# Optimization experiments

Measured on AMD Instinct MI355X. Metric: run time of the kernel, lower is better.

The kernel has to match this reference:

```python
import jax, jax.numpy as jnp
import numpy as np

B, INDIM, ENC, BOT, DEC = 2048, 20000, 512, 128, 512
EPS = 1e-5


def _bn(x, g, b):
    # BatchNorm1d in training mode: biased batch stats
    m = jnp.mean(x, axis=0)
    v = jnp.mean(jnp.square(x - m), axis=0)
    return (x - m) * jax.lax.rsqrt(v + EPS) * g + b


def setup_inputs() -> dict:
    key = jax.random.key(0)
    ks = jax.random.split(key, 8)
    s = 0.02  # small init scale keeps exp() outputs finite
    return {
        "x": jax.random.uniform(ks[0], (B, INDIM), dtype=jnp.float32),
        "bn0_g": jnp.ones((INDIM,), jnp.float32),
        "bn0_b": jnp.zeros((INDIM,), jnp.float32),
        "enc_W": jax.random.normal(ks[1], (ENC, INDIM), jnp.float32) * s,
        "enc_b": jnp.zeros((ENC,), jnp.float32),
        "bn1_g": jnp.ones((ENC,), jnp.float32),
        "bn1_b": jnp.zeros((ENC,), jnp.float32),
        "bot_W": jax.random.normal(ks[2], (BOT, ENC), jnp.float32) * s,
        "bot_b": jnp.zeros((BOT,), jnp.float32),
        "bn2_g": jnp.ones((BOT,), jnp.float32),
        "bn2_b": jnp.zeros((BOT,), jnp.float32),
        "dec_W": jax.random.normal(ks[3], (DEC, BOT), jnp.float32) * s,
        "dec_b": jnp.zeros((DEC,), jnp.float32),
        "o1_W": jax.random.normal(ks[4], (INDIM, DEC), jnp.float32) * s,
        "o1_b": jnp.zeros((INDIM,), jnp.float32),
        "o2_W": jax.random.normal(ks[5], (INDIM, DEC), jnp.float32) * s,
        "o2_b": jnp.zeros((INDIM,), jnp.float32),
        "o3_W": jax.random.normal(ks[6], (INDIM, DEC), jnp.float32) * s,
        "o3_b": jnp.zeros((INDIM,), jnp.float32),
    }


def reference(x, bn0_g, bn0_b, enc_W, enc_b, bn1_g, bn1_b, bot_W, bot_b,
              bn2_g, bn2_b, dec_W, dec_b, o1_W, o1_b, o2_W, o2_b, o3_W, o3_b):
    # row-sum / median normalization; diag-inverse @ x == x / s[:, None]
    row_sum = jnp.sum(x, axis=1)                     # [B]
    s = row_sum / jnp.median(row_sum)                # [B]
    h = jnp.log1p(x / s[:, None])                    # log(inv(diag(s)) @ x + 1)
    h = _bn(h, bn0_g, bn0_b)
    h = jax.nn.relu(h @ enc_W.T + enc_b)
    h = _bn(h, bn1_g, bn1_b)
    h = jax.nn.relu(h @ bot_W.T + bot_b)
    h = _bn(h, bn2_g, bn2_b)
    h = jax.nn.relu(h @ dec_W.T + dec_b)
    M = jnp.exp(h @ o1_W.T + o1_b)
    M_loss = s[:, None] * M                          # diag(s) @ M
    pai = jax.nn.sigmoid(h @ o2_W.T + o2_b)
    theta = jnp.exp(h @ o3_W.T + o3_b)
    return pai, M, theta, M_loss
```

## Files before the change

### kernel.cpp

```cpp
#include <hip/hip_runtime.h>
#include <hip/hip_bf16.h>
#include <math.h>

#define B_    2048
#define IND   20000
#define ENCN  512
#define BOTN  128
#define DECN  512
#define KP1   20480
#define NP    20224
#define SPLITK 16
#define KSTEP1 20
#define BNEPS 1e-5f

typedef __hip_bfloat16 bf16;
typedef __bf16 bf16x8 __attribute__((ext_vector_type(8)));
typedef float f32x4 __attribute__((ext_vector_type(4)));
typedef unsigned short u16;

__device__ __forceinline__ u16 f2bfu(float f) {
  __hip_bfloat16 h = __float2bfloat16(f);
  return *reinterpret_cast<u16*>(&h);
}

__device__ __forceinline__ void gload_lds16(const bf16* g, bf16* l) {
  __builtin_amdgcn_global_load_lds(
      (const __attribute__((address_space(1))) void*)g,
      (__attribute__((address_space(3))) void*)l, 16, 0, 0);
}

__global__ void rowsum_k(const float* __restrict__ x, float* __restrict__ row_sum) {
  const int row = blockIdx.x;
  const f32x4* xr = (const f32x4*)(x + (size_t)row * IND);
  float s = 0.f;
  for (int i = threadIdx.x; i < IND / 4; i += 256) {
    f32x4 v = xr[i];
    s += (v[0] + v[1]) + (v[2] + v[3]);
  }
#pragma unroll
  for (int o = 32; o > 0; o >>= 1) s += __shfl_down(s, o, 64);
  __shared__ float ws4[4];
  if ((threadIdx.x & 63) == 0) ws4[threadIdx.x >> 6] = s;
  __syncthreads();
  if (threadIdx.x == 0) row_sum[row] = (ws4[0] + ws4[1]) + (ws4[2] + ws4[3]);
}

__global__ void median_scale_k(const float* __restrict__ row_sum,
                               float* __restrict__ sArr, float* __restrict__ invs) {
  __shared__ float v[B_];
  const int tid = threadIdx.x;
  v[tid] = row_sum[tid];
  v[tid + 1024] = row_sum[tid + 1024];
  __syncthreads();
  for (int k = 2; k <= B_; k <<= 1) {
    for (int j = k >> 1; j > 0; j >>= 1) {
      for (int i = tid; i < B_; i += 1024) {
        int ixj = i ^ j;
        if (ixj > i) {
          bool up = ((i & k) == 0);
          float a = v[i], b = v[ixj];
          if ((a > b) == up) { v[i] = b; v[ixj] = a; }
        }
      }
      __syncthreads();
    }
  }
  float med = 0.5f * (v[B_ / 2 - 1] + v[B_ / 2]);
  for (int i = tid; i < B_; i += 1024) {
    float rs = row_sum[i];
    sArr[i] = rs / med;
    invs[i] = med / rs;
  }
}

__global__ void pass2_k(const float* __restrict__ x, const float* __restrict__ invs,
                        bf16* __restrict__ L, float* __restrict__ part_s,
                        float* __restrict__ part_q) {
  const int c0 = (blockIdx.x * 256 + threadIdx.x) * 4;
  const int rblk = blockIdx.y;
  const int r0 = rblk * 32;
  const bool valid = (c0 < IND);
  f32x4 sum = {0.f, 0.f, 0.f, 0.f}, sq = {0.f, 0.f, 0.f, 0.f};
  for (int r = r0; r < r0 + 32; ++r) {
    f32x4 lv = {0.f, 0.f, 0.f, 0.f};
    if (valid) {
      f32x4 v = *(const f32x4*)(x + (size_t)r * IND + c0);
      float iv = invs[r];
      lv[0] = log1pf(v[0] * iv); lv[1] = log1pf(v[1] * iv);
      lv[2] = log1pf(v[2] * iv); lv[3] = log1pf(v[3] * iv);
      sum += lv; sq += lv * lv;
    }
    ushort4 o;
    o.x = f2bfu(lv[0]); o.y = f2bfu(lv[1]); o.z = f2bfu(lv[2]); o.w = f2bfu(lv[3]);
    *(ushort4*)((u16*)L + (size_t)r * KP1 + c0) = o;
  }
  if (valid) {
    *(f32x4*)(part_s + (size_t)rblk * KP1 + c0) = sum;
    *(f32x4*)(part_q + (size_t)rblk * KP1 + c0) = sq;
  }
}

__global__ void finalize_bn_k(const float* __restrict__ part_s, const float* __restrict__ part_q,
                              const float* __restrict__ g, const float* __restrict__ b,
                              float* __restrict__ scale, float* __restrict__ shift) {
  int c = blockIdx.x * 256 + threadIdx.x;
  if (c >= IND) return;
  float s = 0.f, q = 0.f;
  for (int z = 0; z < 64; ++z) {
    s += part_s[(size_t)z * KP1 + c];
    q += part_q[(size_t)z * KP1 + c];
  }
  const float invN = 1.f / (float)B_;
  float mean = s * invN;
  float var = q * invN - mean * mean;
  float sc = g[c] * rsqrtf(var + BNEPS);
  scale[c] = sc;
  shift[c] = b[c] - mean * sc;
}

__global__ void prepw_k(const float* __restrict__ encW, const float* __restrict__ enc_b,
                        const float* __restrict__ scale0, const float* __restrict__ shift0,
                        bf16* __restrict__ Wp, float* __restrict__ bias1) {
  const int e = blockIdx.x;
  float local = 0.f;
  for (int j0 = threadIdx.x * 4; j0 < KP1; j0 += 1024) {
    ushort4 o;
    if (j0 < IND) {
      f32x4 w = *(const f32x4*)(encW + (size_t)e * IND + j0);
      f32x4 sc = *(const f32x4*)(scale0 + j0);
      f32x4 sh = *(const f32x4*)(shift0 + j0);
      local += sh[0] * w[0] + sh[1] * w[1] + sh[2] * w[2] + sh[3] * w[3];
      o.x = f2bfu(w[0] * sc[0]); o.y = f2bfu(w[1] * sc[1]);
      o.z = f2bfu(w[2] * sc[2]); o.w = f2bfu(w[3] * sc[3]);
    } else {
      o.x = 0; o.y = 0; o.z = 0; o.w = 0;
    }
    *(ushort4*)((u16*)Wp + (size_t)e * KP1 + j0) = o;
  }
#pragma unroll
  for (int o = 32; o > 0; o >>= 1) local += __shfl_down(local, o, 64);
  __shared__ float red[4];
  if ((threadIdx.x & 63) == 0) red[threadIdx.x >> 6] = local;
  __syncthreads();
  if (threadIdx.x == 0) bias1[e] = enc_b[e] + ((red[0] + red[1]) + (red[2] + red[3]));
}

template <int MODE>
__global__ __launch_bounds__(512, 2)
void gemm256(const bf16* __restrict__ A, const bf16* __restrict__ Bm,
             int Kpad, int ksteps,
             float* __restrict__ out0, float* __restrict__ out1,
             const float* __restrict__ bias, const float* __restrict__ sArr,
             int ldo, int Nlimit) {
  extern __shared__ __align__(16) bf16 smem[];
  bf16* Asm = smem;
  bf16* Bsm = smem + 32768;
  const int tid = threadIdx.x;
  const int lane = tid & 63;
  const int wave = tid >> 6;
  const int wr = wave >> 2;
  const int wc = wave & 3;

  const int nwg = gridDim.x;
  const int q8 = nwg >> 3;
  const int bid = blockIdx.x;
  const int swz = (bid & 7) * q8 + (bid >> 3);
  const int xm = swz & 7;
  const int rest = swz >> 3;
  int yn, z;
  if (MODE == 0) { yn = rest & 1; z = rest >> 1; } else { yn = rest; z = 0; }
  const int m0 = xm * 256;
  const int n0 = yn * 256;
  const int kbeg = z * ksteps * 64;

  const int srow = tid >> 3;
  const int schunk = (tid & 7) ^ (srow & 7);
  const bf16* gA = A + (size_t)(m0 + srow) * Kpad + kbeg + schunk * 8;
  const bf16* gB = Bm + (size_t)(n0 + srow) * Kpad + kbeg + schunk * 8;
  const int dst1 = tid * 8;

  const int lrow = lane & 15;
  const int kq = lane >> 4;
  const int rsw = lrow & 7;

  f32x4 acc[8][4] = {};
  bf16x8 bfv[4][2];

  auto SA = [&](int kt, int half) {
    const bf16* g = gA + (size_t)(half * 128) * Kpad + (size_t)kt * 64;
    bf16* l = Asm + (((kt & 1) * 2 + half) << 13) + dst1;
    gload_lds16(g, l);
    gload_lds16(g + (size_t)64 * Kpad, l + 4096);
  };
  auto SB = [&](int kt, int half) {
    const bf16* g = gB + (size_t)(half * 128) * Kpad + (size_t)kt * 64;
    bf16* l = Bsm + (((kt & 1) * 2 + half) << 13) + dst1;
    gload_lds16(g, l);
    gload_lds16(g + (size_t)64 * Kpad, l + 4096);
  };
  auto DSA = [&](int slot, int p, bf16x8 af[2][2]) {
#pragma unroll
    for (int i = 0; i < 2; ++i) {
      const int m = 2 * p + i;
      const int base = ((slot * 2 + (m >> 2)) * 128 + (m & 3) * 32 + wr * 16 + lrow) * 64;
#pragma unroll
      for (int kk = 0; kk < 2; ++kk)
        af[i][kk] = *(const bf16x8*)(&Asm[base + (((kk * 4 + kq) ^ rsw) << 3)]);
    }
  };
  auto DSB = [&](int slot) {
#pragma unroll
    for (int n = 0; n < 4; ++n) {
      const int base = ((slot * 2 + (wc >> 1)) * 128 + (wc & 1) * 64 + n * 16 + lrow) * 64;
#pragma unroll
      for (int kk = 0; kk < 2; ++kk)
        bfv[n][kk] = *(const bf16x8*)(&Bsm[base + (((kk * 4 + kq) ^ rsw) << 3)]);
    }
  };
  auto MF = [&](int p, bf16x8 af[2][2]) {
    __builtin_amdgcn_s_setprio(1);
#pragma unroll
    for (int i = 0; i < 2; ++i)
#pragma unroll
      for (int n = 0; n < 4; ++n)
#pragma unroll
        for (int kk = 0; kk < 2; ++kk)
          acc[2 * p + i][n] = __builtin_amdgcn_mfma_f32_16x16x32_bf16(
              bfv[n][kk], af[i][kk], acc[2 * p + i][n], 0, 0, 0);
    __builtin_amdgcn_s_setprio(0);
  };

  SA(0, 0); SA(0, 1); SB(0, 0); SB(0, 1);
  SB(1, 0); SB(1, 1); SA(1, 0);
  asm volatile("s_waitcnt vmcnt(6)" ::: "memory");
  __builtin_amdgcn_s_barrier();

  const int iters = ksteps >> 1;
  for (int t = 0; t < iters; ++t) {
    const int e = 2 * t;
    const bool last = (t == iters - 1);
    bf16x8 af[2][2];
    DSB(0); DSA(0, 0, af);
    SA(e + 1, 1);
    __builtin_amdgcn_s_barrier();
    MF(0, af);
    __builtin_amdgcn_s_barrier();
    DSA(0, 1, af);
    if (!last) SB(e + 2, 0);
    __builtin_amdgcn_s_barrier();
    MF(1, af);
    __builtin_amdgcn_s_barrier();
    DSA(0, 2, af);
    if (!last) SB(e + 2, 1);
    __builtin_amdgcn_s_barrier();
    MF(2, af);
    __builtin_amdgcn_s_barrier();
    DSA(0, 3, af);
    if (!last) SA(e + 2, 0);
    if (last) { asm volatile("s_waitcnt vmcnt(0)" ::: "memory"); }
    else      { asm volatile("s_waitcnt vmcnt(6)" ::: "memory"); }
    __builtin_amdgcn_s_barrier();
    MF(3, af);
    __builtin_amdgcn_s_barrier();
    DSB(1); DSA(1, 0, af);
    if (!last) SA(e + 2, 1);
    __builtin_amdgcn_s_barrier();
    MF(0, af);
    __builtin_amdgcn_s_barrier();
    DSA(1, 1, af);
    if (!last) SB(e + 3, 0);
    __builtin_amdgcn_s_barrier();
    MF(1, af);
    __builtin_amdgcn_s_barrier();
    DSA(1, 2, af);
    if (!last) SB(e + 3, 1);
    __builtin_amdgcn_s_barrier();
    MF(2, af);
    __builtin_amdgcn_s_barrier();
    DSA(1, 3, af);
    if (!last) SA(e + 3, 0);
    if (last) { asm volatile("s_waitcnt vmcnt(0)" ::: "memory"); }
    else      { asm volatile("s_waitcnt vmcnt(6)" ::: "memory"); }
    __builtin_amdgcn_s_barrier();
    MF(3, af);
    __builtin_amdgcn_s_barrier();
  }

  float* o0 = out0;
  if (MODE == 0) o0 += (size_t)z * ((size_t)B_ * ldo);
  const int gcolb = n0 + wc * 64 + kq * 4;
#pragma unroll
  for (int m = 0; m < 8; ++m) {
    const int grow = m0 + m * 32 + wr * 16 + lrow;
    float srow_s = 0.f;
    if (MODE == 2) srow_s = sArr[grow];
#pragma unroll
    for (int n = 0; n < 4; ++n) {
      const int gcol = gcolb + n * 16;
      f32x4 v = acc[m][n];
      if (MODE == 0) {
        *(f32x4*)(&o0[(size_t)grow * ldo + gcol]) = v;
      } else if (gcol < Nlimit) {
        f32x4 bb = *(const f32x4*)(&bias[gcol]);
        f32x4 t = v + bb;
        f32x4 r;
        if (MODE == 1) {
#pragma unroll
          for (int j = 0; j < 4; ++j) r[j] = 1.f / (1.f + __expf(-t[j]));
          *(f32x4*)(&o0[(size_t)grow * ldo + gcol]) = r;
        } else if (MODE == 2) {
#pragma unroll
          for (int j = 0; j < 4; ++j) r[j] = __expf(t[j]);
          *(f32x4*)(&o0[(size_t)grow * ldo + gcol]) = r;
          f32x4 rl;
#pragma unroll
          for (int j = 0; j < 4; ++j) rl[j] = srow_s * r[j];
          *(f32x4*)(&out1[(size_t)grow * ldo + gcol]) = rl;
        } else {
#pragma unroll
          for (int j = 0; j < 4; ++j) r[j] = __expf(t[j]);
          *(f32x4*)(&o0[(size_t)grow * ldo + gcol]) = r;
        }
      }
    }
  }
}

template <int MODE>
__global__ __launch_bounds__(256, 2)
void gemm128(const bf16* __restrict__ A, const bf16* __restrict__ Bm,
             int Kpad, int ksteps,
             float* __restrict__ outF, bf16* __restrict__ outB,
             const float* __restrict__ bias, int ldo) {
  __shared__ __align__(16) bf16 As[2][128 * 64];
  __shared__ __align__(16) bf16 Bs[2][128 * 64];
  const int tid = threadIdx.x;
  const int wave = tid >> 6;
  const int lane = tid & 63;
  const int wr = wave >> 1, wc = wave & 1;
  const int m0 = blockIdx.x * 128;
  const int n0 = blockIdx.y * 128;

  const int srow = wave * 32 + (lane >> 3);
  const int scol = ((lane & 7) ^ (lane >> 3)) * 8;
  const bf16* gA = A + (size_t)(m0 + srow) * Kpad + scol;
  const bf16* gB = Bm + (size_t)(n0 + srow) * Kpad + scol;
  const int lbase = wave * 2048;

  f32x4 acc[4][4] = {};
  const int lrow = lane & 15;
  const int swz = lrow & 7;
  const int kq = lane >> 4;

  auto STAGE = [&](int ks, int buf) {
    const bf16* ga = gA + (size_t)ks * 64;
    const bf16* gb = gB + (size_t)ks * 64;
#pragma unroll
    for (int i = 0; i < 4; ++i) {
      gload_lds16(ga + (size_t)(i * 8) * Kpad, &As[buf][lbase + i * 512]);
      gload_lds16(gb + (size_t)(i * 8) * Kpad, &Bs[buf][lbase + i * 512]);
    }
  };

  STAGE(0, 0);
  asm volatile("s_waitcnt vmcnt(0)" ::: "memory");
  __builtin_amdgcn_s_barrier();

  int cur = 0;
  for (int ks = 0; ks < ksteps; ++ks) {
    if (ks + 1 < ksteps) STAGE(ks + 1, cur ^ 1);
#pragma unroll
    for (int kk = 0; kk < 2; ++kk) {
      const int kc = kk * 4 + kq;
      bf16x8 af[4], bfv[4];
#pragma unroll
      for (int m = 0; m < 4; ++m) {
        const int row = wr * 64 + m * 16 + lrow;
        af[m] = *(const bf16x8*)(&As[cur][row * 64 + (((kc ^ swz) & 7) << 3)]);
      }
#pragma unroll
      for (int n = 0; n < 4; ++n) {
        const int row = wc * 64 + n * 16 + lrow;
        bfv[n] = *(const bf16x8*)(&Bs[cur][row * 64 + (((kc ^ swz) & 7) << 3)]);
      }
#pragma unroll
      for (int m = 0; m < 4; ++m)
#pragma unroll
        for (int n = 0; n < 4; ++n)
          acc[m][n] = __builtin_amdgcn_mfma_f32_16x16x32_bf16(bfv[n], af[m], acc[m][n], 0, 0, 0);
    }
    if (ks + 1 < ksteps) {
      asm volatile("s_waitcnt vmcnt(0)" ::: "memory");
      __builtin_amdgcn_s_barrier();
      cur ^= 1;
    }
  }

  const int growb = m0 + wr * 64 + lrow;
  const int gcolb = n0 + wc * 64 + kq * 4;
#pragma unroll
  for (int m = 0; m < 4; ++m) {
    const int grow = growb + m * 16;
#pragma unroll
    for (int n = 0; n < 4; ++n) {
      const int gcol = gcolb + n * 16;
      f32x4 bb = *(const f32x4*)(&bias[gcol]);
      f32x4 t = acc[m][n] + bb;
      if (MODE == 4) {
        f32x4 r;
#pragma unroll
        for (int j = 0; j < 4; ++j) r[j] = fmaxf(t[j], 0.f);
        *(f32x4*)(&outF[(size_t)grow * ldo + gcol]) = r;
      } else {
        ushort4 o;
        o.x = f2bfu(fmaxf(t[0], 0.f)); o.y = f2bfu(fmaxf(t[1], 0.f));
        o.z = f2bfu(fmaxf(t[2], 0.f)); o.w = f2bfu(fmaxf(t[3], 0.f));
        *(ushort4*)((u16*)outB + (size_t)grow * ldo + gcol) = o;
      }
    }
  }
}

__global__ void reduce1_k(const float* __restrict__ Cp, const float* __restrict__ bias1,
                          float* __restrict__ C1) {
  const size_t i4 = ((size_t)blockIdx.x * 256 + threadIdx.x) * 4;
  f32x4 t = {0.f, 0.f, 0.f, 0.f};
#pragma unroll
  for (int z = 0; z < SPLITK; ++z) t += *(const f32x4*)(Cp + (size_t)z * (B_ * ENCN) + i4);
  f32x4 bb = *(const f32x4*)(bias1 + (i4 & (ENCN - 1)));
  t += bb;
  f32x4 r;
#pragma unroll
  for (int j = 0; j < 4; ++j) r[j] = fmaxf(t[j], 0.f);
  *(f32x4*)(C1 + i4) = r;
}

__global__ void colpart_k(const float* __restrict__ X, int C,
                          float* __restrict__ ps, float* __restrict__ pq) {
  const int cl = threadIdx.x & 63;
  const int rg = threadIdx.x >> 6;
  const int c = blockIdx.x * 64 + cl;
  const int r0 = blockIdx.y * 64 + rg * 16;
  float sum = 0.f, sq = 0.f;
  for (int rr = 0; rr < 16; ++rr) {
    float v = X[(size_t)(r0 + rr) * C + c];
    sum += v; sq += v * v;
  }
  __shared__ float ls[4][64], lq[4][64];
  ls[rg][cl] = sum; lq[rg][cl] = sq;
  __syncthreads();
  if (rg == 0) {
    sum = (ls[0][cl] + ls[1][cl]) + (ls[2][cl] + ls[3][cl]);
    sq = (lq[0][cl] + lq[1][cl]) + (lq[2][cl] + lq[3][cl]);
    ps[(size_t)blockIdx.y * C + c] = sum;
    pq[(size_t)blockIdx.y * C + c] = sq;
  }
}

__global__ void colfin_k(const float* __restrict__ ps, const float* __restrict__ pq,
                         const float* __restrict__ g, const float* __restrict__ b,
                         float* __restrict__ scale, float* __restrict__ shift, int C) {
  int c = blockIdx.x * 256 + threadIdx.x;
  if (c >= C) return;
  float sum = 0.f, sq = 0.f;
  for (int z = 0; z < 32; ++z) {
    sum += ps[(size_t)z * C + c];
    sq += pq[(size_t)z * C + c];
  }
  const float invN = 1.f / (float)B_;
  float mean = sum * invN;
  float var = sq * invN - mean * mean;
  float sc = g[c] * rsqrtf(var + BNEPS);
  scale[c] = sc;
  shift[c] = b[c] - mean * sc;
}

__global__ void affine_k(const float* __restrict__ X, const float* __restrict__ sc,
                         const float* __restrict__ sh, bf16* __restrict__ out, int Cm1) {
  const size_t i4 = ((size_t)blockIdx.x * 256 + threadIdx.x) * 4;
  const int c0 = (int)(i4 & (size_t)Cm1);
  f32x4 v = *(const f32x4*)(X + i4);
  f32x4 s = *(const f32x4*)(sc + c0);
  f32x4 h = *(const f32x4*)(sh + c0);
  f32x4 t = v * s + h;
  ushort4 o;
  o.x = f2bfu(t[0]); o.y = f2bfu(t[1]); o.z = f2bfu(t[2]); o.w = f2bfu(t[3]);
  *(ushort4*)((u16*)out + i4) = o;
}

__global__ void cvtw_k(const float* __restrict__ src, bf16* __restrict__ dst) {
  const size_t i4 = ((size_t)blockIdx.x * 256 + threadIdx.x) * 4;
  f32x4 v = *(const f32x4*)(src + i4);
  ushort4 o;
  o.x = f2bfu(v[0]); o.y = f2bfu(v[1]); o.z = f2bfu(v[2]); o.w = f2bfu(v[3]);
  *(ushort4*)((u16*)dst + i4) = o;
}

__global__ void cvt_o_k(const float* __restrict__ Wsrc, bf16* __restrict__ Wb) {
  const size_t idx = ((size_t)blockIdx.x * 256 + threadIdx.x) * 4;
  const int e = (int)(idx >> 9);
  ushort4 o;
  if (e < IND) {
    f32x4 v = *(const f32x4*)(Wsrc + idx);
    o.x = f2bfu(v[0]); o.y = f2bfu(v[1]); o.z = f2bfu(v[2]); o.w = f2bfu(v[3]);
  } else {
    o.x = 0; o.y = 0; o.z = 0; o.w = 0;
  }
  *(ushort4*)((u16*)Wb + idx) = o;
}

extern "C" void kernel_launch(void* const* d_in, const int* in_sizes, int n_in,
                              void* d_out, int out_size, void* d_ws, size_t ws_size,
                              hipStream_t stream) {
  const float* x     = (const float*)d_in[0];
  const float* bn0_g = (const float*)d_in[1];
  const float* bn0_b = (const float*)d_in[2];
  const float* enc_W = (const float*)d_in[3];
  const float* enc_b = (const float*)d_in[4];
  const float* bn1_g = (const float*)d_in[5];
  const float* bn1_b = (const float*)d_in[6];
  const float* bot_W = (const float*)d_in[7];
  const float* bot_b = (const float*)d_in[8];
  const float* bn2_g = (const float*)d_in[9];
  const float* bn2_b = (const float*)d_in[10];
  const float* dec_W = (const float*)d_in[11];
  const float* dec_b = (const float*)d_in[12];
  const float* o1_W  = (const float*)d_in[13];
  const float* o1_b  = (const float*)d_in[14];
  const float* o2_W  = (const float*)d_in[15];
  const float* o2_b  = (const float*)d_in[16];
  const float* o3_W  = (const float*)d_in[17];
  const float* o3_b  = (const float*)d_in[18];

  char* wsb = (char*)d_ws;
  size_t off = 0;
  auto alloc = [&](size_t bytes) -> void* {
    void* p = wsb + off;
    off = (off + bytes + 255) & ~(size_t)255;
    return p;
  };
  float* row_sum = (float*)alloc(B_ * 4);
  float* sArr    = (float*)alloc(B_ * 4);
  float* invs    = (float*)alloc(B_ * 4);
  float* scale0  = (float*)alloc(IND * 4);
  float* shift0  = (float*)alloc(IND * 4);
  float* bias1   = (float*)alloc(ENCN * 4);
  float* scale1  = (float*)alloc(ENCN * 4);
  float* shift1  = (float*)alloc(ENCN * 4);
  float* scale2  = (float*)alloc(BOTN * 4);
  float* shift2  = (float*)alloc(BOTN * 4);
  float* ps1     = (float*)alloc(32 * ENCN * 4);
  float* pq1     = (float*)alloc(32 * ENCN * 4);
  float* ps2     = (float*)alloc(32 * BOTN * 4);
  float* pq2     = (float*)alloc(32 * BOTN * 4);
  float* C1      = (float*)alloc((size_t)B_ * ENCN * 4);
  float* C2f     = (float*)alloc((size_t)B_ * BOTN * 4);
  float* Cp      = (float*)alloc((size_t)SPLITK * B_ * ENCN * 4);
  bf16*  L       = (bf16*)alloc((size_t)B_ * KP1 * 2);
  bf16*  Wp      = (bf16*)alloc((size_t)ENCN * KP1 * 2);
  bf16*  A1b     = (bf16*)alloc((size_t)B_ * ENCN * 2);
  bf16*  A2b     = (bf16*)alloc((size_t)B_ * BOTN * 2);
  bf16*  botWb   = (bf16*)alloc((size_t)BOTN * ENCN * 2);
  bf16*  decWb   = (bf16*)alloc((size_t)DECN * BOTN * 2);
  bf16*  h3      = (bf16*)alloc((size_t)B_ * DECN * 2);
  bf16*  wbf0    = (bf16*)alloc((size_t)NP * 512 * 2);
  bf16*  wbf1    = (bf16*)alloc((size_t)NP * 512 * 2);
  bf16*  wbf2    = (bf16*)alloc((size_t)NP * 512 * 2);
  float* part_s  = Cp;
  float* part_q  = Cp + (size_t)64 * KP1;

  hipFuncSetAttribute(reinterpret_cast<const void*>(gemm256<0>),
                      hipFuncAttributeMaxDynamicSharedMemorySize, 131072);
  hipFuncSetAttribute(reinterpret_cast<const void*>(gemm256<1>),
                      hipFuncAttributeMaxDynamicSharedMemorySize, 131072);
  hipFuncSetAttribute(reinterpret_cast<const void*>(gemm256<2>),
                      hipFuncAttributeMaxDynamicSharedMemorySize, 131072);
  hipFuncSetAttribute(reinterpret_cast<const void*>(gemm256<3>),
                      hipFuncAttributeMaxDynamicSharedMemorySize, 131072);

  rowsum_k<<<B_, 256, 0, stream>>>(x, row_sum);
  median_scale_k<<<1, 1024, 0, stream>>>(row_sum, sArr, invs);

  pass2_k<<<dim3(KP1 / 1024, 64), 256, 0, stream>>>(x, invs, L, part_s, part_q);
  finalize_bn_k<<<(IND + 255) / 256, 256, 0, stream>>>(part_s, part_q, bn0_g, bn0_b,
                                                       scale0, shift0);

  prepw_k<<<ENCN, 256, 0, stream>>>(enc_W, enc_b, scale0, shift0, Wp, bias1);

  gemm256<0><<<8 * 2 * SPLITK, 512, 131072, stream>>>(
      L, Wp, KP1, KSTEP1, Cp, nullptr, nullptr, nullptr, ENCN, ENCN);
  reduce1_k<<<(B_ * ENCN) / 1024, 256, 0, stream>>>(Cp, bias1, C1);

  colpart_k<<<dim3(ENCN / 64, 32), 256, 0, stream>>>(C1, ENCN, ps1, pq1);
  colfin_k<<<2, 256, 0, stream>>>(ps1, pq1, bn1_g, bn1_b, scale1, shift1, ENCN);
  affine_k<<<(B_ * ENCN) / 1024, 256, 0, stream>>>(C1, scale1, shift1, A1b, ENCN - 1);
  cvtw_k<<<(BOTN * ENCN) / 1024, 256, 0, stream>>>(bot_W, botWb);
  gemm128<4><<<dim3(16, 1), 256, 0, stream>>>(A1b, botWb, ENCN, ENCN / 64,
                                              C2f, nullptr, bot_b, BOTN);
  colpart_k<<<dim3(BOTN / 64, 32), 256, 0, stream>>>(C2f, BOTN, ps2, pq2);
  colfin_k<<<1, 256, 0, stream>>>(ps2, pq2, bn2_g, bn2_b, scale2, shift2, BOTN);
  affine_k<<<(B_ * BOTN) / 1024, 256, 0, stream>>>(C2f, scale2, shift2, A2b, BOTN - 1);
  cvtw_k<<<(DECN * BOTN) / 1024, 256, 0, stream>>>(dec_W, decWb);
  gemm128<5><<<dim3(16, 4), 256, 0, stream>>>(A2b, decWb, BOTN, BOTN / 64,
                                              nullptr, h3, dec_b, DECN);

  const int cvtg = (NP * 512) / 1024;
  cvt_o_k<<<cvtg, 256, 0, stream>>>(o1_W, wbf0);
  cvt_o_k<<<cvtg, 256, 0, stream>>>(o2_W, wbf1);
  cvt_o_k<<<cvtg, 256, 0, stream>>>(o3_W, wbf2);

  float* out = (float*)d_out;
  const size_t OFF = (size_t)B_ * IND;
  const int onwg = 8 * (NP / 256);
  gemm256<1><<<onwg, 512, 131072, stream>>>(
      h3, wbf1, 512, 8, out, nullptr, o2_b, nullptr, IND, IND);
  gemm256<2><<<onwg, 512, 131072, stream>>>(
      h3, wbf0, 512, 8, out + OFF, out + 3 * OFF, o1_b, sArr, IND, IND);
  gemm256<3><<<onwg, 512, 131072, stream>>>(
      h3, wbf2, 512, 8, out + 2 * OFF, nullptr, o3_b, nullptr, IND, IND);
}
```

Baseline: 670.8 us.

## Fuse three output GEMMs into one persistent kernel with cross-tile prefetch

Result: slower. 710.0 us (+5.8%).

```diff
diff --git a/kernel.cpp b/kernel.cpp
--- a/kernel.cpp
+++ b/kernel.cpp
@@ -145,13 +145,9 @@
   if (threadIdx.x == 0) bias1[e] = enc_b[e] + ((red[0] + red[1]) + (red[2] + red[3]));
 }
 
-template <int MODE>
 __global__ __launch_bounds__(512, 2)
-void gemm256(const bf16* __restrict__ A, const bf16* __restrict__ Bm,
-             int Kpad, int ksteps,
-             float* __restrict__ out0, float* __restrict__ out1,
-             const float* __restrict__ bias, const float* __restrict__ sArr,
-             int ldo, int Nlimit) {
+void gemm1_k(const bf16* __restrict__ A, const bf16* __restrict__ Bm,
+             float* __restrict__ Cp) {
   extern __shared__ __align__(16) bf16 smem[];
   bf16* Asm = smem;
   bf16* Bsm = smem + 32768;
@@ -161,22 +157,20 @@
   const int wr = wave >> 2;
   const int wc = wave & 3;
 
-  const int nwg = gridDim.x;
-  const int q8 = nwg >> 3;
   const int bid = blockIdx.x;
-  const int swz = (bid & 7) * q8 + (bid >> 3);
+  const int swz = (bid & 7) * 32 + (bid >> 3);
   const int xm = swz & 7;
   const int rest = swz >> 3;
-  int yn, z;
-  if (MODE == 0) { yn = rest & 1; z = rest >> 1; } else { yn = rest; z = 0; }
+  const int yn = rest & 1;
+  const int z = rest >> 1;
   const int m0 = xm * 256;
   const int n0 = yn * 256;
-  const int kbeg = z * ksteps * 64;
+  const int kbeg = z * KSTEP1 * 64;
 
   const int srow = tid >> 3;
   const int schunk = (tid & 7) ^ (srow & 7);
-  const bf16* gA = A + (size_t)(m0 + srow) * Kpad + kbeg + schunk * 8;
-  const bf16* gB = Bm + (size_t)(n0 + srow) * Kpad + kbeg + schunk * 8;
+  const bf16* gA = A + (size_t)(m0 + srow) * KP1 + kbeg + schunk * 8;
+  const bf16* gB = Bm + (size_t)(n0 + srow) * KP1 + kbeg + schunk * 8;
   const int dst1 = tid * 8;
 
   const int lrow = lane & 15;
@@ -187,16 +181,16 @@
   bf16x8 bfv[4][2];
 
   auto SA = [&](int kt, int half) {
-    const bf16* g = gA + (size_t)(half * 128) * Kpad + (size_t)kt * 64;
+    const bf16* g = gA + (size_t)(half * 128) * KP1 + (size_t)kt * 64;
     bf16* l = Asm + (((kt & 1) * 2 + half) << 13) + dst1;
     gload_lds16(g, l);
-    gload_lds16(g + (size_t)64 * Kpad, l + 4096);
+    gload_lds16(g + (size_t)64 * KP1, l + 4096);
   };
   auto SB = [&](int kt, int half) {
-    const bf16* g = gB + (size_t)(half * 128) * Kpad + (size_t)kt * 64;
+    const bf16* g = gB + (size_t)(half * 128) * KP1 + (size_t)kt * 64;
     bf16* l = Bsm + (((kt & 1) * 2 + half) << 13) + dst1;
     gload_lds16(g, l);
-    gload_lds16(g + (size_t)64 * Kpad, l + 4096);
+    gload_lds16(g + (size_t)64 * KP1, l + 4096);
   };
   auto DSA = [&](int slot, int p, bf16x8 af[2][2]) {
 #pragma unroll
@@ -235,7 +229,7 @@
   asm volatile("s_waitcnt vmcnt(6)" ::: "memory");
   __builtin_amdgcn_s_barrier();
 
-  const int iters = ksteps >> 1;
+  const int iters = KSTEP1 >> 1;
   for (int t = 0; t < iters; ++t) {
     const int e = 2 * t;
     const bool last = (t == iters - 1);
@@ -286,42 +280,220 @@
     __builtin_amdgcn_s_barrier();
   }
 
-  float* o0 = out0;
-  if (MODE == 0) o0 += (size_t)z * ((size_t)B_ * ldo);
+  float* o0 = Cp + (size_t)z * ((size_t)B_ * ENCN);
   const int gcolb = n0 + wc * 64 + kq * 4;
 #pragma unroll
   for (int m = 0; m < 8; ++m) {
     const int grow = m0 + m * 32 + wr * 16 + lrow;
-    float srow_s = 0.f;
-    if (MODE == 2) srow_s = sArr[grow];
 #pragma unroll
     for (int n = 0; n < 4; ++n) {
       const int gcol = gcolb + n * 16;
-      f32x4 v = acc[m][n];
-      if (MODE == 0) {
-        *(f32x4*)(&o0[(size_t)grow * ldo + gcol]) = v;
-      } else if (gcol < Nlimit) {
-        f32x4 bb = *(const f32x4*)(&bias[gcol]);
-        f32x4 t = v + bb;
-        f32x4 r;
-        if (MODE == 1) {
-#pragma unroll
-          for (int j = 0; j < 4; ++j) r[j] = 1.f / (1.f + __expf(-t[j]));
-          *(f32x4*)(&o0[(size_t)grow * ldo + gcol]) = r;
-        } else if (MODE == 2) {
-#pragma unroll
-          for (int j = 0; j < 4; ++j) r[j] = __expf(t[j]);
-          *(f32x4*)(&o0[(size_t)grow * ldo + gcol]) = r;
-          f32x4 rl;
-#pragma unroll
-          for (int j = 0; j < 4; ++j) rl[j] = srow_s * r[j];
-          *(f32x4*)(&out1[(size_t)grow * ldo + gcol]) = rl;
-        } else {
-#pragma unroll
-          for (int j = 0; j < 4; ++j) r[j] = __expf(t[j]);
-          *(f32x4*)(&o0[(size_t)grow * ldo + gcol]) = r;
+      *(f32x4*)(&o0[(size_t)grow * ENCN + gcol]) = acc[m][n];
+    }
+  }
+}
+
+__global__ __launch_bounds__(512, 2)
+void gemm_outp_k(const bf16* __restrict__ A,
+                 const bf16* __restrict__ W0, const bf16* __restrict__ W1,
+                 const bf16* __restrict__ W2,
+                 const float* __restrict__ b0, const float* __restrict__ b1,
+                 const float* __restrict__ b2,
+                 const float* __restrict__ sArr, float* __restrict__ out) {
+  extern __shared__ __align__(16) bf16 smem[];
+  bf16* Asm = smem;
+  bf16* Bsm = smem + 32768;
+  const int tid = threadIdx.x;
+  const int lane = tid & 63;
+  const int wave = tid >> 6;
+  const int wr = wave >> 2;
+  const int wc = wave & 3;
+
+  const int bid = blockIdx.x;
+  const int c = bid & 7;
+  const int j = bid >> 3;
+  const int nt = (j < 13) ? 8 : 7;
+
+  const int srow = tid >> 3;
+  const int schunk = (tid & 7) ^ (srow & 7);
+  const int dst1 = tid * 8;
+  const int lrow = lane & 15;
+  const int kq = lane >> 4;
+  const int rsw = lrow & 7;
+  const size_t OFF = (size_t)B_ * IND;
+
+  const int xm = (c * 237 + j) & 7;
+  const int m0 = xm * 256;
+  const bf16* gA = A + (size_t)(m0 + srow) * ENCN + schunk * 8;
+
+  auto tileParams = [&](int it, int& g, int& yn) {
+    const int tg = c * 237 + j + 32 * it;
+    g = tg / 632;
+    yn = (tg - g * 632) >> 3;
+  };
+  auto wsel = [&](int g) -> const bf16* { return (g == 0) ? W0 : (g == 1) ? W1 : W2; };
+
+  int g_cur, yn_cur;
+  tileParams(0, g_cur, yn_cur);
+  const bf16* gB_cur = wsel(g_cur) + (size_t)(yn_cur * 256 + srow) * ENCN + schunk * 8;
+  int g_nxt = 0, yn_nxt = 0;
+  const bf16* gB_nxt = gB_cur;
+  if (nt > 1) {
+    tileParams(1, g_nxt, yn_nxt);
+    gB_nxt = wsel(g_nxt) + (size_t)(yn_nxt * 256 + srow) * ENCN + schunk * 8;
+  }
+
+  f32x4 acc[8][4] = {};
+  bf16x8 bfv[4][2];
+
+  auto SA = [&](int kt, int half) {
+    const bf16* g = gA + (size_t)(half * 128) * ENCN + (size_t)(kt & 7) * 64;
+    bf16* l = Asm + (((kt & 1) * 2 + half) << 13) + dst1;
+    gload_lds16(g, l);
+    gload_lds16(g + (size_t)64 * ENCN, l + 4096);
+  };
+  auto SB = [&](int kt, int half) {
+    const bf16* base = (kt >= 8) ? gB_nxt : gB_cur;
+    const bf16* g = base + (size_t)(half * 128) * ENCN + (size_t)(kt & 7) * 64;
+    bf16* l = Bsm + (((kt & 1) * 2 + half) << 13) + dst1;
+    gload_lds16(g, l);
+    gload_lds16(g + (size_t)64 * ENCN, l + 4096);
+  };
+  auto DSA = [&](int slot, int p, bf16x8 af[2][2]) {
+#pragma unroll
+    for (int i = 0; i < 2; ++i) {
+      const int m = 2 * p + i;
+      const int base = ((slot * 2 + (m >> 2)) * 128 + (m & 3) * 32 + wr * 16 + lrow) * 64;
+#pragma unroll
+      for (int kk = 0; kk < 2; ++kk)
+        af[i][kk] = *(const bf16x8*)(&Asm[base + (((kk * 4 + kq) ^ rsw) << 3)]);
+    }
+  };
+  auto DSB = [&](int slot) {
+#pragma unroll
+    for (int n = 0; n < 4; ++n) {
+      const int base = ((slot * 2 + (wc >> 1)) * 128 + (wc & 1) * 64 + n * 16 + lrow) * 64;
+#pragma unroll
+      for (int kk = 0; kk < 2; ++kk)
+        bfv[n][kk] = *(const bf16x8*)(&Bsm[base + (((kk * 4 + kq) ^ rsw) << 3)]);
+    }
+  };
+  auto MF = [&](int p, bf16x8 af[2][2]) {
+    __builtin_amdgcn_s_setprio(1);
+#pragma unroll
+    for (int i = 0; i < 2; ++i)
+#pragma unroll
+      for (int n = 0; n < 4; ++n)
+#pragma unroll
+        for (int kk = 0; kk < 2; ++kk)
+          acc[2 * p + i][n] = __builtin_amdgcn_mfma_f32_16x16x32_bf16(
+              bfv[n][kk], af[i][kk], acc[2 * p + i][n], 0, 0, 0);
+    __builtin_amdgcn_s_setprio(0);
+  };
+
+  SA(0, 0); SA(0, 1); SB(0, 0); SB(0, 1);
+  SB(1, 0); SB(1, 1); SA(1, 0);
+  asm volatile("s_waitcnt vmcnt(6)" ::: "memory");
+  __builtin_amdgcn_s_barrier();
+
+  for (int it = 0; it < nt; ++it) {
+    const bool lastTile = (it == nt - 1);
+#pragma unroll 1
+    for (int t = 0; t < 4; ++t) {
+      const int e = 2 * t;
+      const bool last = lastTile && (t == 3);
+      bf16x8 af[2][2];
+      DSB(0); DSA(0, 0, af);
+      SA(e + 1, 1);
+      __builtin_amdgcn_s_barrier();
+      MF(0, af);
+      __builtin_amdgcn_s_barrier();
+      DSA(0, 1, af);
+      if (!last) SB(e + 2, 0);
+      __builtin_amdgcn_s_barrier();
+      MF(1, af);
+      __builtin_amdgcn_s_barrier();
+      DSA(0, 2, af);
+      if (!last) SB(e + 2, 1);
+      __builtin_amdgcn_s_barrier();
+      MF(2, af);
+      __builtin_amdgcn_s_barrier();
+      DSA(0, 3, af);
+      if (!last) SA(e + 2, 0);
+      if (last) { asm volatile("s_waitcnt vmcnt(0)" ::: "memory"); }
+      else      { asm volatile("s_waitcnt vmcnt(6)" ::: "memory"); }
+      __builtin_amdgcn_s_barrier();
+      MF(3, af);
+      __builtin_amdgcn_s_barrier();
+      DSB(1); DSA(1, 0, af);
+      if (!last) SA(e + 2, 1);
+      __builtin_amdgcn_s_barrier();
+      MF(0, af);
+      __builtin_amdgcn_s_barrier();
+      DSA(1, 1, af);
+      if (!last) SB(e + 3, 0);
+      __builtin_amdgcn_s_barrier();
+      MF(1, af);
+      __builtin_amdgcn_s_barrier();
+      DSA(1, 2, af);
+      if (!last) SB(e + 3, 1);
+      __builtin_amdgcn_s_barrier();
+      MF(2, af);
+      __builtin_amdgcn_s_barrier();
+      DSA(1, 3, af);
+      if (!last) SA(e + 3, 0);
+      if (last) { asm volatile("s_waitcnt vmcnt(0)" ::: "memory"); }
+      else      { asm volatile("s_waitcnt vmcnt(6)" ::: "memory"); }
+      __builtin_amdgcn_s_barrier();
+      MF(3, af);
+      __builtin_amdgcn_s_barrier();
+    }
+
+    {
+      const int g = g_cur;
+      const int n0 = yn_cur * 256;
+      const float* bg = (g == 0) ? b0 : (g == 1) ? b1 : b2;
+      float* o0 = out + (size_t)g * OFF;
+      float* o1 = out + 3 * OFF;
+      const int gcolb = n0 + wc * 64 + kq * 4;
+#pragma unroll
+      for (int m = 0; m < 8; ++m) {
+        const int grow = m0 + m * 32 + wr * 16 + lrow;
+        float ss = 0.f;
+        if (g == 1) ss = sArr[grow];
+#pragma unroll
+        for (int n = 0; n < 4; ++n) {
+          const int gcol = gcolb + n * 16;
+          f32x4 v = acc[m][n];
+          acc[m][n] = f32x4{0.f, 0.f, 0.f, 0.f};
+          if (gcol < IND) {
+            f32x4 bb = *(const f32x4*)(&bg[gcol]);
+            f32x4 tt = v + bb;
+            f32x4 r;
+            if (g == 0) {
+#pragma unroll
+              for (int q = 0; q < 4; ++q) r[q] = 1.f / (1.f + __expf(-tt[q]));
+              *(f32x4*)(&o0[(size_t)grow * IND + gcol]) = r;
+            } else {
+#pragma unroll
+              for (int q = 0; q < 4; ++q) r[q] = __expf(tt[q]);
+              *(f32x4*)(&o0[(size_t)grow * IND + gcol]) = r;
+              if (g == 1) {
+                f32x4 rl;
+#pragma unroll
+                for (int q = 0; q < 4; ++q) rl[q] = ss * r[q];
+                *(f32x4*)(&o1[(size_t)grow * IND + gcol]) = rl;
+              }
+            }
+          }
         }
       }
+    }
+
+    g_cur = g_nxt; yn_cur = yn_nxt; gB_cur = gB_nxt;
+    if (it + 2 < nt) {
+      tileParams(it + 2, g_nxt, yn_nxt);
+      gB_nxt = wsel(g_nxt) + (size_t)(yn_nxt * 256 + srow) * ENCN + schunk * 8;
     }
   }
 }
@@ -569,13 +741,9 @@
   float* part_s  = Cp;
   float* part_q  = Cp + (size_t)64 * KP1;
 
-  hipFuncSetAttribute(reinterpret_cast<const void*>(gemm256<0>),
+  hipFuncSetAttribute(reinterpret_cast<const void*>(gemm1_k),
                       hipFuncAttributeMaxDynamicSharedMemorySize, 131072);
-  hipFuncSetAttribute(reinterpret_cast<const void*>(gemm256<1>),
-                      hipFuncAttributeMaxDynamicSharedMemorySize, 131072);
-  hipFuncSetAttribute(reinterpret_cast<const void*>(gemm256<2>),
-                      hipFuncAttributeMaxDynamicSharedMemorySize, 131072);
-  hipFuncSetAttribute(reinterpret_cast<const void*>(gemm256<3>),
+  hipFuncSetAttribute(reinterpret_cast<const void*>(gemm_outp_k),
                       hipFuncAttributeMaxDynamicSharedMemorySize, 131072);
 
   rowsum_k<<<B_, 256, 0, stream>>>(x, row_sum);
@@ -587,8 +755,7 @@
 
   prepw_k<<<ENCN, 256, 0, stream>>>(enc_W, enc_b, scale0, shift0, Wp, bias1);
 
-  gemm256<0><<<8 * 2 * SPLITK, 512, 131072, stream>>>(
-      L, Wp, KP1, KSTEP1, Cp, nullptr, nullptr, nullptr, ENCN, ENCN);
+  gemm1_k<<<256, 512, 131072, stream>>>(L, Wp, Cp);
   reduce1_k<<<(B_ * ENCN) / 1024, 256, 0, stream>>>(Cp, bias1, C1);
 
   colpart_k<<<dim3(ENCN / 64, 32), 256, 0, stream>>>(C1, ENCN, ps1, pq1);
@@ -610,12 +777,6 @@
   cvt_o_k<<<cvtg, 256, 0, stream>>>(o3_W, wbf2);
 
   float* out = (float*)d_out;
-  const size_t OFF = (size_t)B_ * IND;
-  const int onwg = 8 * (NP / 256);
-  gemm256<1><<<onwg, 512, 131072, stream>>>(
-      h3, wbf1, 512, 8, out, nullptr, o2_b, nullptr, IND, IND);
-  gemm256<2><<<onwg, 512, 131072, stream>>>(
-      h3, wbf0, 512, 8, out + OFF, out + 3 * OFF, o1_b, sArr, IND, IND);
-  gemm256<3><<<onwg, 512, 131072, stream>>>(
-      h3, wbf2, 512, 8, out + 2 * OFF, nullptr, o3_b, nullptr, IND, IND);
-}
+  gemm_outp_k<<<256, 512, 131072, stream>>>(h3, wbf1, wbf0, wbf2,
+                                            o2_b, o1_b, o3_b, sArr, out);
+}
```

## Use dedicated 128x128 tiled GEMM for output heads and specialize encoder GEMM

Applied to the files above, without the earlier changes.

Result: slower. 736.0 us (+9.7%).

```diff
diff --git a/kernel.cpp b/kernel.cpp
--- a/kernel.cpp
+++ b/kernel.cpp
@@ -145,13 +145,9 @@
   if (threadIdx.x == 0) bias1[e] = enc_b[e] + ((red[0] + red[1]) + (red[2] + red[3]));
 }
 
-template <int MODE>
 __global__ __launch_bounds__(512, 2)
-void gemm256(const bf16* __restrict__ A, const bf16* __restrict__ Bm,
-             int Kpad, int ksteps,
-             float* __restrict__ out0, float* __restrict__ out1,
-             const float* __restrict__ bias, const float* __restrict__ sArr,
-             int ldo, int Nlimit) {
+void gemm1_k(const bf16* __restrict__ A, const bf16* __restrict__ Bm,
+             float* __restrict__ Cp) {
   extern __shared__ __align__(16) bf16 smem[];
   bf16* Asm = smem;
   bf16* Bsm = smem + 32768;
@@ -161,22 +157,20 @@
   const int wr = wave >> 2;
   const int wc = wave & 3;
 
-  const int nwg = gridDim.x;
-  const int q8 = nwg >> 3;
   const int bid = blockIdx.x;
-  const int swz = (bid & 7) * q8 + (bid >> 3);
+  const int swz = (bid & 7) * 32 + (bid >> 3);
   const int xm = swz & 7;
   const int rest = swz >> 3;
-  int yn, z;
-  if (MODE == 0) { yn = rest & 1; z = rest >> 1; } else { yn = rest; z = 0; }
+  const int yn = rest & 1;
+  const int z = rest >> 1;
   const int m0 = xm * 256;
   const int n0 = yn * 256;
-  const int kbeg = z * ksteps * 64;
+  const int kbeg = z * KSTEP1 * 64;
 
   const int srow = tid >> 3;
   const int schunk = (tid & 7) ^ (srow & 7);
-  const bf16* gA = A + (size_t)(m0 + srow) * Kpad + kbeg + schunk * 8;
-  const bf16* gB = Bm + (size_t)(n0 + srow) * Kpad + kbeg + schunk * 8;
+  const bf16* gA = A + (size_t)(m0 + srow) * KP1 + kbeg + schunk * 8;
+  const bf16* gB = Bm + (size_t)(n0 + srow) * KP1 + kbeg + schunk * 8;
   const int dst1 = tid * 8;
 
   const int lrow = lane & 15;
@@ -187,16 +181,16 @@
   bf16x8 bfv[4][2];
 
   auto SA = [&](int kt, int half) {
-    const bf16* g = gA + (size_t)(half * 128) * Kpad + (size_t)kt * 64;
+    const bf16* g = gA + (size_t)(half * 128) * KP1 + (size_t)kt * 64;
     bf16* l = Asm + (((kt & 1) * 2 + half) << 13) + dst1;
     gload_lds16(g, l);
-    gload_lds16(g + (size_t)64 * Kpad, l + 4096);
+    gload_lds16(g + (size_t)64 * KP1, l + 4096);
   };
   auto SB = [&](int kt, int half) {
-    const bf16* g = gB + (size_t)(half * 128) * Kpad + (size_t)kt * 64;
+    const bf16* g = gB + (size_t)(half * 128) * KP1 + (size_t)kt * 64;
     bf16* l = Bsm + (((kt & 1) * 2 + half) << 13) + dst1;
     gload_lds16(g, l);
-    gload_lds16(g + (size_t)64 * Kpad, l + 4096);
+    gload_lds16(g + (size_t)64 * KP1, l + 4096);
   };
   auto DSA = [&](int slot, int p, bf16x8 af[2][2]) {
 #pragma unroll
@@ -235,7 +229,7 @@
   asm volatile("s_waitcnt vmcnt(6)" ::: "memory");
   __builtin_amdgcn_s_barrier();
 
-  const int iters = ksteps >> 1;
+  const int iters = KSTEP1 >> 1;
   for (int t = 0; t < iters; ++t) {
     const int e = 2 * t;
     const bool last = (t == iters - 1);
@@ -286,40 +280,118 @@
     __builtin_amdgcn_s_barrier();
   }
 
-  float* o0 = out0;
-  if (MODE == 0) o0 += (size_t)z * ((size_t)B_ * ldo);
+  float* o0 = Cp + (size_t)z * ((size_t)B_ * ENCN);
   const int gcolb = n0 + wc * 64 + kq * 4;
 #pragma unroll
   for (int m = 0; m < 8; ++m) {
     const int grow = m0 + m * 32 + wr * 16 + lrow;
+#pragma unroll
+    for (int n = 0; n < 4; ++n) {
+      const int gcol = gcolb + n * 16;
+      *(f32x4*)(&o0[(size_t)grow * ENCN + gcol]) = acc[m][n];
+    }
+  }
+}
+
+template <int MODE>
+__global__ __launch_bounds__(256, 2)
+void gemm_bt(const bf16* __restrict__ A, const bf16* __restrict__ Bm,
+             float* __restrict__ out0, float* __restrict__ out1,
+             const float* __restrict__ bias, const float* __restrict__ sArr) {
+  __shared__ __align__(16) bf16 As[2][128 * 64];
+  __shared__ __align__(16) bf16 Bs[2][128 * 64];
+  const int tid = threadIdx.x;
+  const int wave = tid >> 6;
+  const int lane = tid & 63;
+  const int wr = wave >> 1, wc = wave & 1;
+  const int m0 = blockIdx.x * 128;
+  const int n0 = blockIdx.y * 128;
+
+  const int srow = wave * 32 + (lane >> 3);
+  const int scol = ((lane & 7) ^ (lane >> 3)) * 8;
+  const bf16* gA = A + (size_t)(m0 + srow) * ENCN + scol;
+  const bf16* gB = Bm + (size_t)(n0 + srow) * ENCN + scol;
+  const int lbase = wave * 2048;
+
+  f32x4 acc[4][4] = {};
+  const int lrow = lane & 15;
+  const int swz = lrow & 7;
+  const int kq = lane >> 4;
+
+  auto STAGE = [&](int ks, int buf) {
+    const bf16* ga = gA + (size_t)ks * 64;
+    const bf16* gb = gB + (size_t)ks * 64;
+#pragma unroll
+    for (int i = 0; i < 4; ++i) {
+      gload_lds16(ga + (size_t)(i * 8) * ENCN, &As[buf][lbase + i * 512]);
+      gload_lds16(gb + (size_t)(i * 8) * ENCN, &Bs[buf][lbase + i * 512]);
+    }
+  };
+
+  STAGE(0, 0);
+  asm volatile("s_waitcnt vmcnt(0)" ::: "memory");
+  __builtin_amdgcn_s_barrier();
+
+  int cur = 0;
+  for (int ks = 0; ks < 8; ++ks) {
+    if (ks + 1 < 8) STAGE(ks + 1, cur ^ 1);
+#pragma unroll
+    for (int kk = 0; kk < 2; ++kk) {
+      const int kc = kk * 4 + kq;
+      bf16x8 af[4], bfv[4];
+#pragma unroll
+      for (int m = 0; m < 4; ++m) {
+        const int row = wr * 64 + m * 16 + lrow;
+        af[m] = *(const bf16x8*)(&As[cur][row * 64 + (((kc ^ swz) & 7) << 3)]);
+      }
+#pragma unroll
+      for (int n = 0; n < 4; ++n) {
+        const int row = wc * 64 + n * 16 + lrow;
+        bfv[n] = *(const bf16x8*)(&Bs[cur][row * 64 + (((kc ^ swz) & 7) << 3)]);
+      }
+#pragma unroll
+      for (int m = 0; m < 4; ++m)
+#pragma unroll
+        for (int n = 0; n < 4; ++n)
+          acc[m][n] = __builtin_amdgcn_mfma_f32_16x16x32_bf16(bfv[n], af[m], acc[m][n], 0, 0, 0);
+    }
+    if (ks + 1 < 8) {
+      asm volatile("s_waitcnt vmcnt(0)" ::: "memory");
+      __builtin_amdgcn_s_barrier();
+      cur ^= 1;
+    }
+  }
+
+  const int growb = m0 + wr * 64 + lrow;
+  const int gcolb = n0 + wc * 64 + kq * 4;
+#pragma unroll
+  for (int m = 0; m < 4; ++m) {
+    const int grow = growb + m * 16;
     float srow_s = 0.f;
     if (MODE == 2) srow_s = sArr[grow];
 #pragma unroll
     for (int n = 0; n < 4; ++n) {
       const int gcol = gcolb + n * 16;
-      f32x4 v = acc[m][n];
-      if (MODE == 0) {
-        *(f32x4*)(&o0[(size_t)grow * ldo + gcol]) = v;
-      } else if (gcol < Nlimit) {
+      if (gcol < IND) {
         f32x4 bb = *(const f32x4*)(&bias[gcol]);
-        f32x4 t = v + bb;
+        f32x4 t = acc[m][n] + bb;
         f32x4 r;
         if (MODE == 1) {
 #pragma unroll
           for (int j = 0; j < 4; ++j) r[j] = 1.f / (1.f + __expf(-t[j]));
-          *(f32x4*)(&o0[(size_t)grow * ldo + gcol]) = r;
+          *(f32x4*)(&out0[(size_t)grow * IND + gcol]) = r;
         } else if (MODE == 2) {
 #pragma unroll
           for (int j = 0; j < 4; ++j) r[j] = __expf(t[j]);
-          *(f32x4*)(&o0[(size_t)grow * ldo + gcol]) = r;
+          *(f32x4*)(&out0[(size_t)grow * IND + gcol]) = r;
           f32x4 rl;
 #pragma unroll
           for (int j = 0; j < 4; ++j) rl[j] = srow_s * r[j];
-          *(f32x4*)(&out1[(size_t)grow * ldo + gcol]) = rl;
+          *(f32x4*)(&out1[(size_t)grow * IND + gcol]) = rl;
         } else {
 #pragma unroll
           for (int j = 0; j < 4; ++j) r[j] = __expf(t[j]);
-          *(f32x4*)(&o0[(size_t)grow * ldo + gcol]) = r;
+          *(f32x4*)(&out0[(size_t)grow * IND + gcol]) = r;
         }
       }
     }
@@ -569,13 +641,7 @@
   float* part_s  = Cp;
   float* part_q  = Cp + (size_t)64 * KP1;
 
-  hipFuncSetAttribute(reinterpret_cast<const void*>(gemm256<0>),
-                      hipFuncAttributeMaxDynamicSharedMemorySize, 131072);
-  hipFuncSetAttribute(reinterpret_cast<const void*>(gemm256<1>),
-                      hipFuncAttributeMaxDynamicSharedMemorySize, 131072);
-  hipFuncSetAttribute(reinterpret_cast<const void*>(gemm256<2>),
-                      hipFuncAttributeMaxDynamicSharedMemorySize, 131072);
-  hipFuncSetAttribute(reinterpret_cast<const void*>(gemm256<3>),
+  hipFuncSetAttribute(reinterpret_cast<const void*>(gemm1_k),
                       hipFuncAttributeMaxDynamicSharedMemorySize, 131072);
 
   rowsum_k<<<B_, 256, 0, stream>>>(x, row_sum);
@@ -587,8 +653,7 @@
 
   prepw_k<<<ENCN, 256, 0, stream>>>(enc_W, enc_b, scale0, shift0, Wp, bias1);
 
-  gemm256<0><<<8 * 2 * SPLITK, 512, 131072, stream>>>(
-      L, Wp, KP1, KSTEP1, Cp, nullptr, nullptr, nullptr, ENCN, ENCN);
+  gemm1_k<<<256, 512, 131072, stream>>>(L, Wp, Cp);
   reduce1_k<<<(B_ * ENCN) / 1024, 256, 0, stream>>>(Cp, bias1, C1);
 
   colpart_k<<<dim3(ENCN / 64, 32), 256, 0, stream>>>(C1, ENCN, ps1, pq1);
@@ -611,11 +676,8 @@
 
   float* out = (float*)d_out;
   const size_t OFF = (size_t)B_ * IND;
-  const int onwg = 8 * (NP / 256);
-  gemm256<1><<<onwg, 512, 131072, stream>>>(
-      h3, wbf1, 512, 8, out, nullptr, o2_b, nullptr, IND, IND);
-  gemm256<2><<<onwg, 512, 131072, stream>>>(
-      h3, wbf0, 512, 8, out + OFF, out + 3 * OFF, o1_b, sArr, IND, IND);
-  gemm256<3><<<onwg, 512, 131072, stream>>>(
-      h3, wbf2, 512, 8, out + 2 * OFF, nullptr, o3_b, nullptr, IND, IND);
-}
+  const dim3 ogrid(B_ / 128, NP / 128);
+  gemm_bt<1><<<ogrid, 256, 0, stream>>>(h3, wbf1, out, nullptr, o2_b, nullptr);
+  gemm_bt<2><<<ogrid, 256, 0, stream>>>(h3, wbf0, out + OFF, out + 3 * OFF, o1_b, sArr);
+  gemm_bt<3><<<ogrid, 256, 0, stream>>>(h3, wbf2, out + 2 * OFF, nullptr, o3_b, nullptr);
+}
```
